# Kernel tuning notes

Measured on AMD Instinct MI355X. Metric: run time of the kernel, lower is better.

Reference implementation:

```python
import jax, jax.numpy as jnp
import numpy as np

B, T, D, H = 4, 2048, 1024, 16
HD = D // H  # head dim = 64


def setup_inputs() -> dict:
    key = jax.random.key(0)
    ks = jax.random.split(key, 6)
    s = 0.02
    return {
        "x": jax.random.normal(ks[0], (B, T, D), dtype=jnp.float32),
        "Wk": jax.random.normal(ks[1], (D, D), dtype=jnp.float32) * s,
        "Wq": jax.random.normal(ks[2], (D, D), dtype=jnp.float32) * s,
        "Wv": jax.random.normal(ks[3], (D, D), dtype=jnp.float32) * s,
        "Wp": jax.random.normal(ks[4], (D, D), dtype=jnp.float32) * s,
        "bp": jnp.zeros((D,), dtype=jnp.float32),
    }


def reference(x, Wk, Wq, Wv, Wp, bp):
    # nn.Linear applies x @ W.T; weights here are stored torch-style [out, in]
    Bq, Tq, _ = x.shape
    k = (x @ Wk.T).reshape(Bq, Tq, H, HD).transpose(0, 2, 1, 3)  # [B,H,T,hd]
    q = (x @ Wq.T).reshape(Bq, Tq, H, HD).transpose(0, 2, 1, 3)
    v = (x @ Wv.T).reshape(Bq, Tq, H, HD).transpose(0, 2, 1, 3)
    scale = HD ** -0.5
    attn = jnp.einsum('bhqd,bhkd->bhqk', q, k) * scale  # [B,H,T,T]
    causal = jnp.tril(jnp.ones((Tq, Tq), dtype=bool))
    attn = jnp.where(causal, attn, -jnp.inf)
    attn = jax.nn.softmax(attn, axis=-1)
    # dropout p=0.0 -> identity (eval semantics)
    out = jnp.einsum('bhqk,bhkd->bhqd', attn, v)  # [B,H,T,hd]
    out = out.transpose(0, 2, 1, 3).reshape(Bq, Tq, D)
    return out @ Wp.T + bp
```

## Files before the change

### kernel.cpp

```cpp
#include <hip/hip_runtime.h>
#include <hip/hip_bf16.h>
#include <stdint.h>


typedef __bf16 bf16x8 __attribute__((ext_vector_type(8)));
typedef float floatx4 __attribute__((ext_vector_type(4)));
typedef unsigned short ushort_t;
typedef unsigned short ushortx8 __attribute__((ext_vector_type(8)));
typedef unsigned short ushortx4 __attribute__((ext_vector_type(4)));

#define MFMA16(a, b, c) __builtin_amdgcn_mfma_f32_16x16x32_bf16((a), (b), (c), 0, 0, 0)

static __device__ __forceinline__ ushort_t f2bfu(float f) {
  union { float f; unsigned u; } v; v.f = f;
  unsigned r = v.u + 0x7FFFu + ((v.u >> 16) & 1u);
  return (ushort_t)(r >> 16);
}

static __device__ __forceinline__ void gl_lds16(const void* g, void* l) {
  __builtin_amdgcn_global_load_lds(
      (const __attribute__((address_space(1))) void*)g,
      (__attribute__((address_space(3))) void*)l, 16, 0, 0);
}

__global__ void cvt_kernel(const float* __restrict__ in, ushort_t* __restrict__ out, int n4) {
  int i = blockIdx.x * blockDim.x + threadIdx.x;
  if (i >= n4) return;
  const float4 f = reinterpret_cast<const float4*>(in)[i];
  ushortx4 o;
  o[0] = f2bfu(f.x); o[1] = f2bfu(f.y); o[2] = f2bfu(f.z); o[3] = f2bfu(f.w);
  reinterpret_cast<ushortx4*>(out)[i] = o;
}

__global__ __launch_bounds__(256) void gemm_qkv(
    const ushort_t* __restrict__ X,
    const ushort_t* __restrict__ Wq, const ushort_t* __restrict__ Wk,
    const ushort_t* __restrict__ Wv,
    ushort_t* __restrict__ qb, ushort_t* __restrict__ kb, ushort_t* __restrict__ vtb)
{
  const int z = blockIdx.z;
  const ushort_t* Bm = (z == 0) ? Wq : (z == 1) ? Wk : Wv;
  __shared__ ushort_t Al[128 * 64];
  __shared__ ushort_t Bl[128 * 64];
  const int tid = threadIdx.x;
  const int w = tid >> 6, lane = tid & 63, g = lane >> 4, c = lane & 15;
  const int wm = w >> 1, wn = w & 1;
  const int cswz = c & 7;
  const int m0 = blockIdx.x * 128, n0 = blockIdx.y * 128;

  floatx4 acc[4][4];
  const floatx4 zero4 = {0.f, 0.f, 0.f, 0.f};
#pragma unroll
  for (int i = 0; i < 4; ++i)
#pragma unroll
    for (int j = 0; j < 4; ++j) acc[i][j] = zero4;

  const int srow = tid >> 3;
  const int gsw  = ((tid & 7) ^ (srow & 7)) * 8;

  for (int k0 = 0; k0 < 1024; k0 += 64) {
#pragma unroll
    for (int p = 0; p < 4; ++p) {
      const int row = p * 32 + srow;
      gl_lds16(&X [(size_t)(m0 + row) * 1024 + k0 + gsw], &Al[p * 2048 + tid * 8]);
      gl_lds16(&Bm[(size_t)(n0 + row) * 1024 + k0 + gsw], &Bl[p * 2048 + tid * 8]);
    }
    __syncthreads();
#pragma unroll
    for (int kk = 0; kk < 2; ++kk) {
      bf16x8 af[4], bfr[4];
#pragma unroll
      for (int i = 0; i < 4; ++i) {
        const int sw = ((kk * 4 + g) ^ cswz) * 8;
        af[i]  = *reinterpret_cast<const bf16x8*>(&Al[(wm * 64 + i * 16 + c) * 64 + sw]);
        bfr[i] = *reinterpret_cast<const bf16x8*>(&Bl[(wn * 64 + i * 16 + c) * 64 + sw]);
      }
#pragma unroll
      for (int i = 0; i < 4; ++i)
#pragma unroll
        for (int j = 0; j < 4; ++j)
          acc[i][j] = MFMA16(af[i], bfr[j], acc[i][j]);
    }
    __syncthreads();
  }

#pragma unroll
  for (int i = 0; i < 4; ++i) {
#pragma unroll
    for (int j = 0; j < 4; ++j) {
      const int mbase = m0 + wm * 64 + i * 16 + g * 4;
      const int n = n0 + wn * 64 + j * 16 + c;
      const int h = n >> 6, d = n & 63;
      if (z == 2) {
        const int bb = mbase >> 11, t = mbase & 2047;
        ushortx4 pk;
#pragma unroll
        for (int r = 0; r < 4; ++r) pk[r] = f2bfu(acc[i][j][r]);
        *reinterpret_cast<ushortx4*>(&vtb[(size_t)((bb * 16 + h) * 64 + d) * 2048 + t]) = pk;
      } else {
        ushort_t* ob = (z == 0) ? qb : kb;
#pragma unroll
        for (int r = 0; r < 4; ++r) {
          const int m = mbase + r;
          const int bb = m >> 11, t = m & 2047;
          ob[(size_t)((bb * 16 + h) * 2048 + t) * 64 + d] = f2bfu(acc[i][j][r]);
        }
      }
    }
  }
}

__global__ __launch_bounds__(256) void attn_kernel(
    const ushort_t* __restrict__ qbuf, const ushort_t* __restrict__ kbuf,
    const ushort_t* __restrict__ vtbuf, ushort_t* __restrict__ obuf)
{
  const int j = blockIdx.x, h = blockIdx.y, b = blockIdx.z;
  const int tid = threadIdx.x, w = tid >> 6, lane = tid & 63, g = lane >> 4, c = lane & 15;
  const int cswz = c & 7;

  __shared__ ushort_t Kl[64 * 64];
  __shared__ ushort_t Vl[64 * 64];
  __shared__ ushort_t Pl[4][2][16 * 72];

  const size_t bh = (size_t)(b * 16 + h);
  const ushort_t* kb_bh = kbuf + bh * 2048 * 64;
  const ushort_t* vt_bh = vtbuf + bh * 64 * 2048;

  const int rb0 = j * 64 + w * 16;
  const int rb1 = (31 - j) * 64 + w * 16;

  bf16x8 aq0[2], aq1[2];
  {
    const ushort_t* qp0 = qbuf + (bh * 2048 + rb0 + c) * 64;
    aq0[0] = *reinterpret_cast<const bf16x8*>(qp0 + g * 8);
    aq0[1] = *reinterpret_cast<const bf16x8*>(qp0 + 32 + g * 8);
    const ushort_t* qp1 = qbuf + (bh * 2048 + rb1 + c) * 64;
    aq1[0] = *reinterpret_cast<const bf16x8*>(qp1 + g * 8);
    aq1[1] = *reinterpret_cast<const bf16x8*>(qp1 + 32 + g * 8);
  }

  floatx4 oacc0[4], oacc1[4];
  float lp0[4], lp1[4];
  const floatx4 zero4 = {0.f, 0.f, 0.f, 0.f};
#pragma unroll
  for (int td = 0; td < 4; ++td) { oacc0[td] = zero4; oacc1[td] = zero4; }
#pragma unroll
  for (int r = 0; r < 4; ++r) { lp0[r] = 0.f; lp1[r] = 0.f; }

  const int drow = tid >> 3;
  const int gsw  = ((tid & 7) ^ (drow & 7)) * 8;

  const int ktlast = 31 - j;
  for (int kt = 0; kt <= ktlast; ++kt) {
    const int key0 = kt * 64;
#pragma unroll
    for (int p = 0; p < 2; ++p) {
      const int r = p * 32 + drow;
      gl_lds16(&kb_bh[(size_t)(key0 + r) * 64 + gsw], &Kl[p * 2048 + tid * 8]);
      gl_lds16(&vt_bh[(size_t)r * 2048 + key0 + gsw], &Vl[p * 2048 + tid * 8]);
    }
    __syncthreads();

#pragma unroll
    for (int grp = 0; grp < 2; ++grp) {
      if (grp == 0 && kt > j) continue;
      const int rb = (grp == 0) ? rb0 : rb1;
      const int dg = (grp == 0) ? j : 31 - j;
      const bf16x8 a0 = (grp == 0) ? aq0[0] : aq1[0];
      const bf16x8 a1 = (grp == 0) ? aq0[1] : aq1[1];
      float pv[4][4];
#pragma unroll
      for (int t4 = 0; t4 < 4; ++t4) {
        const int krow = (t4 * 16 + c) * 64;
        const bf16x8 k0f = *reinterpret_cast<const bf16x8*>(&Kl[krow + ((g) ^ cswz) * 8]);
        const bf16x8 k1f = *reinterpret_cast<const bf16x8*>(&Kl[krow + ((4 + g) ^ cswz) * 8]);
        floatx4 sa = zero4;
        sa = MFMA16(a0, k0f, sa);
        sa = MFMA16(a1, k1f, sa);
        if (kt == dg) {
          const int key = key0 + t4 * 16 + c;
#pragma unroll
          for (int r = 0; r < 4; ++r) {
            const float e = __expf(sa[r] * 0.125f);
            pv[t4][r] = (key <= rb + g * 4 + r) ? e : 0.f;
          }
        } else {
#pragma unroll
          for (int r = 0; r < 4; ++r) pv[t4][r] = __expf(sa[r] * 0.125f);
        }
      }
#pragma unroll
      for (int r = 0; r < 4; ++r) {
        const float s = (pv[0][r] + pv[1][r]) + (pv[2][r] + pv[3][r]);
        if (grp == 0) lp0[r] += s; else lp1[r] += s;
      }

      ushort_t* pw = Pl[w][grp];
#pragma unroll
      for (int t4 = 0; t4 < 4; ++t4)
#pragma unroll
        for (int r = 0; r < 4; ++r)
          pw[(g * 4 + r) * 72 + t4 * 16 + c] = f2bfu(pv[t4][r]);
      const bf16x8 ap0 = *reinterpret_cast<const bf16x8*>(&pw[c * 72 + g * 8]);
      const bf16x8 ap1 = *reinterpret_cast<const bf16x8*>(&pw[c * 72 + 32 + g * 8]);
#pragma unroll
      for (int td = 0; td < 4; ++td) {
        const int vrow = (td * 16 + c) * 64;
        const bf16x8 bv0 = *reinterpret_cast<const bf16x8*>(&Vl[vrow + ((g) ^ cswz) * 8]);
        const bf16x8 bv1 = *reinterpret_cast<const bf16x8*>(&Vl[vrow + ((4 + g) ^ cswz) * 8]);
        if (grp == 0) {
          oacc0[td] = MFMA16(ap0, bv0, oacc0[td]);
          oacc0[td] = MFMA16(ap1, bv1, oacc0[td]);
        } else {
          oacc1[td] = MFMA16(ap0, bv0, oacc1[td]);
          oacc1[td] = MFMA16(ap1, bv1, oacc1[td]);
        }
      }
    }
    __syncthreads();
  }

#pragma unroll
  for (int grp = 0; grp < 2; ++grp) {
    const int rb = (grp == 0) ? rb0 : rb1;
#pragma unroll
    for (int r = 0; r < 4; ++r) {
      float ls = (grp == 0) ? lp0[r] : lp1[r];
#pragma unroll
      for (int o = 1; o < 16; o <<= 1) ls += __shfl_xor(ls, o, 64);
      const float inv = 1.f / ls;
      const int q = rb + g * 4 + r;
#pragma unroll
      for (int td = 0; td < 4; ++td) {
        const int d = td * 16 + c;
        const float ov = ((grp == 0) ? oacc0[td][r] : oacc1[td][r]) * inv;
        obuf[((size_t)(b * 2048 + q) * 16 + h) * 64 + d] = f2bfu(ov);
      }
    }
  }
}

__global__ __launch_bounds__(256) void gemm_proj(
    const ushort_t* __restrict__ A, const ushort_t* __restrict__ Wp,
    const float* __restrict__ bias, float* __restrict__ out)
{
  __shared__ ushort_t Al[128 * 64];
  __shared__ ushort_t Bl[128 * 64];
  const int tid = threadIdx.x;
  const int w = tid >> 6, lane = tid & 63, g = lane >> 4, c = lane & 15;
  const int wm = w >> 1, wn = w & 1;
  const int cswz = c & 7;
  const int m0 = blockIdx.x * 128, n0 = blockIdx.y * 128;

  floatx4 acc[4][4];
  const floatx4 zero4 = {0.f, 0.f, 0.f, 0.f};
#pragma unroll
  for (int i = 0; i < 4; ++i)
#pragma unroll
    for (int j = 0; j < 4; ++j) acc[i][j] = zero4;

  const int srow = tid >> 3;
  const int gsw  = ((tid & 7) ^ (srow & 7)) * 8;

  for (int k0 = 0; k0 < 1024; k0 += 64) {
#pragma unroll
    for (int p = 0; p < 4; ++p) {
      const int row = p * 32 + srow;
      gl_lds16(&A [(size_t)(m0 + row) * 1024 + k0 + gsw], &Al[p * 2048 + tid * 8]);
      gl_lds16(&Wp[(size_t)(n0 + row) * 1024 + k0 + gsw], &Bl[p * 2048 + tid * 8]);
    }
    __syncthreads();
#pragma unroll
    for (int kk = 0; kk < 2; ++kk) {
      bf16x8 af[4], bfr[4];
#pragma unroll
      for (int i = 0; i < 4; ++i) {
        const int sw = ((kk * 4 + g) ^ cswz) * 8;
        af[i]  = *reinterpret_cast<const bf16x8*>(&Al[(wm * 64 + i * 16 + c) * 64 + sw]);
        bfr[i] = *reinterpret_cast<const bf16x8*>(&Bl[(wn * 64 + i * 16 + c) * 64 + sw]);
      }
#pragma unroll
      for (int i = 0; i < 4; ++i)
#pragma unroll
        for (int j = 0; j < 4; ++j)
          acc[i][j] = MFMA16(af[i], bfr[j], acc[i][j]);
    }
    __syncthreads();
  }

#pragma unroll
  for (int i = 0; i < 4; ++i) {
#pragma unroll
    for (int j = 0; j < 4; ++j) {
      const int n = n0 + wn * 64 + j * 16 + c;
      const float bv = bias[n];
#pragma unroll
      for (int r = 0; r < 4; ++r) {
        const int m = m0 + wm * 64 + i * 16 + g * 4 + r;
        out[(size_t)m * 1024 + n] = acc[i][j][r] + bv;
      }
    }
  }
}

extern "C" void kernel_launch(void* const* d_in, const int* in_sizes, int n_in,
                              void* d_out, int out_size, void* d_ws, size_t ws_size,
                              hipStream_t stream) {
  const float* x  = (const float*)d_in[0];
  const float* Wk = (const float*)d_in[1];
  const float* Wq = (const float*)d_in[2];
  const float* Wv = (const float*)d_in[3];
  const float* Wp = (const float*)d_in[4];
  const float* bp = (const float*)d_in[5];
  float* out = (float*)d_out;

  char* ws = (char*)d_ws;
  const size_t SZ_X = (size_t)8192 * 1024 * 2;
  const size_t SZ_W = (size_t)1024 * 1024 * 2;
  ushort_t* xb    = (ushort_t*)ws;  ws += SZ_X;
  ushort_t* wkb   = (ushort_t*)ws;  ws += SZ_W;
  ushort_t* wqb   = (ushort_t*)ws;  ws += SZ_W;
  ushort_t* wvb   = (ushort_t*)ws;  ws += SZ_W;
  ushort_t* wpb   = (ushort_t*)ws;  ws += SZ_W;
  ushort_t* qbuf  = (ushort_t*)ws;  ws += SZ_X;
  ushort_t* kbuf  = (ushort_t*)ws;  ws += SZ_X;
  ushort_t* vtbuf = (ushort_t*)ws;  ws += SZ_X;
  ushort_t* obuf  = xb;

  cvt_kernel<<<8192, 256, 0, stream>>>(x,  xb,  8192 * 1024 / 4);
  cvt_kernel<<<1024, 256, 0, stream>>>(Wk, wkb, 1024 * 1024 / 4);
  cvt_kernel<<<1024, 256, 0, stream>>>(Wq, wqb, 1024 * 1024 / 4);
  cvt_kernel<<<1024, 256, 0, stream>>>(Wv, wvb, 1024 * 1024 / 4);
  cvt_kernel<<<1024, 256, 0, stream>>>(Wp, wpb, 1024 * 1024 / 4);

  gemm_qkv<<<dim3(64, 8, 3), 256, 0, stream>>>(xb, wqb, wkb, wvb, qbuf, kbuf, vtbuf);
  attn_kernel<<<dim3(16, 16, 4), 256, 0, stream>>>(qbuf, kbuf, vtbuf, obuf);
  gemm_proj<<<dim3(64, 8), 256, 0, stream>>>(obuf, wpb, bp, out);
}
```

Baseline: 280.6 us.

## Fuse conversions, widen attention key tiles, store Q transposed, truncate P

The five float-to-bf16 conversion launches become one kernel that writes into the contiguous workspace. The attention loop now stages 128-key K/V tiles per barrier instead of 64, which halves the number of synchronizations, and it shares a single P scratch buffer per wave. Q is written transposed by the QKV GEMM with vectorized stores and gathered element-wise in attention. P is converted to bf16 by truncation rather than rounding, which slightly reduces accuracy, and the larger tiles use more LDS.

```diff
diff --git a/kernel.cpp b/kernel.cpp
--- a/kernel.cpp
+++ b/kernel.cpp
@@ -16,6 +16,10 @@
   unsigned r = v.u + 0x7FFFu + ((v.u >> 16) & 1u);
   return (ushort_t)(r >> 16);
 }
+static __device__ __forceinline__ ushort_t f2bfu_trunc(float f) {
+  union { float f; unsigned u; } v; v.f = f;
+  return (ushort_t)(v.u >> 16);
+}
 
 static __device__ __forceinline__ void gl_lds16(const void* g, void* l) {
   __builtin_amdgcn_global_load_lds(
@@ -23,20 +27,29 @@
       (__attribute__((address_space(3))) void*)l, 16, 0, 0);
 }
 
-__global__ void cvt_kernel(const float* __restrict__ in, ushort_t* __restrict__ out, int n4) {
-  int i = blockIdx.x * blockDim.x + threadIdx.x;
-  if (i >= n4) return;
-  const float4 f = reinterpret_cast<const float4*>(in)[i];
+__global__ void cvt_all(const float* __restrict__ x,  const float* __restrict__ wk,
+                        const float* __restrict__ wq, const float* __restrict__ wv,
+                        const float* __restrict__ wp, ushortx4* __restrict__ dst) {
+  const int i = blockIdx.x * blockDim.x + threadIdx.x;
+  const float4* src; int off;
+  if (i < 2097152) { src = (const float4*)x; off = i; }
+  else {
+    const int r = i - 2097152;
+    const int sel = r >> 18;
+    off = r & 262143;
+    src = (const float4*)(sel == 0 ? wk : sel == 1 ? wq : sel == 2 ? wv : wp);
+  }
+  const float4 f = src[off];
   ushortx4 o;
   o[0] = f2bfu(f.x); o[1] = f2bfu(f.y); o[2] = f2bfu(f.z); o[3] = f2bfu(f.w);
-  reinterpret_cast<ushortx4*>(out)[i] = o;
+  dst[i] = o;
 }
 
 __global__ __launch_bounds__(256) void gemm_qkv(
     const ushort_t* __restrict__ X,
     const ushort_t* __restrict__ Wq, const ushort_t* __restrict__ Wk,
     const ushort_t* __restrict__ Wv,
-    ushort_t* __restrict__ qb, ushort_t* __restrict__ kb, ushort_t* __restrict__ vtb)
+    ushort_t* __restrict__ qtb, ushort_t* __restrict__ kb, ushort_t* __restrict__ vtb)
 {
   const int z = blockIdx.z;
   const ushort_t* Bm = (z == 0) ? Wq : (z == 1) ? Wk : Wv;
@@ -91,19 +104,19 @@
       const int mbase = m0 + wm * 64 + i * 16 + g * 4;
       const int n = n0 + wn * 64 + j * 16 + c;
       const int h = n >> 6, d = n & 63;
-      if (z == 2) {
+      if (z != 1) {
+        ushort_t* ob = (z == 0) ? qtb : vtb;
         const int bb = mbase >> 11, t = mbase & 2047;
         ushortx4 pk;
 #pragma unroll
         for (int r = 0; r < 4; ++r) pk[r] = f2bfu(acc[i][j][r]);
-        *reinterpret_cast<ushortx4*>(&vtb[(size_t)((bb * 16 + h) * 64 + d) * 2048 + t]) = pk;
+        *reinterpret_cast<ushortx4*>(&ob[(size_t)((bb * 16 + h) * 64 + d) * 2048 + t]) = pk;
       } else {
-        ushort_t* ob = (z == 0) ? qb : kb;
 #pragma unroll
         for (int r = 0; r < 4; ++r) {
           const int m = mbase + r;
           const int bb = m >> 11, t = m & 2047;
-          ob[(size_t)((bb * 16 + h) * 2048 + t) * 64 + d] = f2bfu(acc[i][j][r]);
+          kb[(size_t)((bb * 16 + h) * 2048 + t) * 64 + d] = f2bfu(acc[i][j][r]);
         }
       }
     }
@@ -111,32 +124,36 @@
 }
 
 __global__ __launch_bounds__(256) void attn_kernel(
-    const ushort_t* __restrict__ qbuf, const ushort_t* __restrict__ kbuf,
+    const ushort_t* __restrict__ qtbuf, const ushort_t* __restrict__ kbuf,
     const ushort_t* __restrict__ vtbuf, ushort_t* __restrict__ obuf)
 {
   const int j = blockIdx.x, h = blockIdx.y, b = blockIdx.z;
   const int tid = threadIdx.x, w = tid >> 6, lane = tid & 63, g = lane >> 4, c = lane & 15;
-  const int cswz = c & 7;
-
-  __shared__ ushort_t Kl[64 * 64];
-  __shared__ ushort_t Vl[64 * 64];
-  __shared__ ushort_t Pl[4][2][16 * 72];
+
+  __shared__ ushort_t Kl[128 * 64];
+  __shared__ ushort_t Vl[64 * 128];
+  __shared__ ushort_t Pl[4][16 * 72];
 
   const size_t bh = (size_t)(b * 16 + h);
   const ushort_t* kb_bh = kbuf + bh * 2048 * 64;
   const ushort_t* vt_bh = vtbuf + bh * 64 * 2048;
+  const ushort_t* qt_bh = qtbuf + bh * 64 * 2048;
 
   const int rb0 = j * 64 + w * 16;
   const int rb1 = (31 - j) * 64 + w * 16;
 
   bf16x8 aq0[2], aq1[2];
   {
-    const ushort_t* qp0 = qbuf + (bh * 2048 + rb0 + c) * 64;
-    aq0[0] = *reinterpret_cast<const bf16x8*>(qp0 + g * 8);
-    aq0[1] = *reinterpret_cast<const bf16x8*>(qp0 + 32 + g * 8);
-    const ushort_t* qp1 = qbuf + (bh * 2048 + rb1 + c) * 64;
-    aq1[0] = *reinterpret_cast<const bf16x8*>(qp1 + g * 8);
-    aq1[1] = *reinterpret_cast<const bf16x8*>(qp1 + 32 + g * 8);
+    union { ushortx8 u; bf16x8 v; } t00, t01, t10, t11;
+#pragma unroll
+    for (int jj = 0; jj < 8; ++jj) {
+      const int d0 = g * 8 + jj, d1 = 32 + g * 8 + jj;
+      t00.u[jj] = qt_bh[(size_t)d0 * 2048 + rb0 + c];
+      t01.u[jj] = qt_bh[(size_t)d1 * 2048 + rb0 + c];
+      t10.u[jj] = qt_bh[(size_t)d0 * 2048 + rb1 + c];
+      t11.u[jj] = qt_bh[(size_t)d1 * 2048 + rb1 + c];
+    }
+    aq0[0] = t00.v; aq0[1] = t01.v; aq1[0] = t10.v; aq1[1] = t11.v;
   }
 
   floatx4 oacc0[4], oacc1[4];
@@ -147,73 +164,82 @@
 #pragma unroll
   for (int r = 0; r < 4; ++r) { lp0[r] = 0.f; lp1[r] = 0.f; }
 
-  const int drow = tid >> 3;
-  const int gsw  = ((tid & 7) ^ (drow & 7)) * 8;
-
-  const int ktlast = 31 - j;
-  for (int kt = 0; kt <= ktlast; ++kt) {
-    const int key0 = kt * 64;
-#pragma unroll
-    for (int p = 0; p < 2; ++p) {
-      const int r = p * 32 + drow;
-      gl_lds16(&kb_bh[(size_t)(key0 + r) * 64 + gsw], &Kl[p * 2048 + tid * 8]);
-      gl_lds16(&vt_bh[(size_t)r * 2048 + key0 + gsw], &Vl[p * 2048 + tid * 8]);
-    }
-    __syncthreads();
-
-#pragma unroll
-    for (int grp = 0; grp < 2; ++grp) {
-      if (grp == 0 && kt > j) continue;
-      const int rb = (grp == 0) ? rb0 : rb1;
-      const int dg = (grp == 0) ? j : 31 - j;
-      const bf16x8 a0 = (grp == 0) ? aq0[0] : aq1[0];
-      const bf16x8 a1 = (grp == 0) ? aq0[1] : aq1[1];
-      float pv[4][4];
-#pragma unroll
-      for (int t4 = 0; t4 < 4; ++t4) {
-        const int krow = (t4 * 16 + c) * 64;
-        const bf16x8 k0f = *reinterpret_cast<const bf16x8*>(&Kl[krow + ((g) ^ cswz) * 8]);
-        const bf16x8 k1f = *reinterpret_cast<const bf16x8*>(&Kl[krow + ((4 + g) ^ cswz) * 8]);
-        floatx4 sa = zero4;
-        sa = MFMA16(a0, k0f, sa);
-        sa = MFMA16(a1, k1f, sa);
-        if (kt == dg) {
-          const int key = key0 + t4 * 16 + c;
-#pragma unroll
-          for (int r = 0; r < 4; ++r) {
-            const float e = __expf(sa[r] * 0.125f);
-            pv[t4][r] = (key <= rb + g * 4 + r) ? e : 0.f;
+  const int krow_s = tid >> 3;
+  const int kgsw   = ((tid & 7) ^ (krow_s & 7)) * 8;
+  const int vrow_s = tid >> 4;
+  const int vgsw   = ((tid & 15) ^ (vrow_s & 15)) * 8;
+
+  const int n128 = (33 - j) >> 1;
+  for (int kt = 0; kt < n128; ++kt) {
+    const int key0 = kt * 128;
+#pragma unroll
+    for (int p = 0; p < 4; ++p) {
+      const int kr = p * 32 + krow_s;
+      gl_lds16(&kb_bh[(size_t)(key0 + kr) * 64 + kgsw], &Kl[p * 2048 + tid * 8]);
+      const int vr = p * 16 + vrow_s;
+      gl_lds16(&vt_bh[(size_t)vr * 2048 + key0 + vgsw], &Vl[p * 2048 + tid * 8]);
+    }
+    __syncthreads();
+
+#pragma unroll
+    for (int s = 0; s < 2; ++s) {
+      const int ti = 2 * kt + s;
+      const int key0s = ti * 64;
+#pragma unroll
+      for (int grp = 0; grp < 2; ++grp) {
+        const int lim = (grp == 0) ? j : 31 - j;
+        if (ti > lim) continue;
+        const int rb = (grp == 0) ? rb0 : rb1;
+        const bf16x8 a0 = (grp == 0) ? aq0[0] : aq1[0];
+        const bf16x8 a1 = (grp == 0) ? aq0[1] : aq1[1];
+
+        float pv[4][4];
+#pragma unroll
+        for (int t4 = 0; t4 < 4; ++t4) {
+          const int krow = s * 64 + t4 * 16 + c;
+          const bf16x8 k0f = *reinterpret_cast<const bf16x8*>(&Kl[krow * 64 + ((g) ^ (c & 7)) * 8]);
+          const bf16x8 k1f = *reinterpret_cast<const bf16x8*>(&Kl[krow * 64 + ((4 + g) ^ (c & 7)) * 8]);
+          floatx4 sa = zero4;
+          sa = MFMA16(a0, k0f, sa);
+          sa = MFMA16(a1, k1f, sa);
+          if (ti == lim) {
+            const int key = key0s + t4 * 16 + c;
+#pragma unroll
+            for (int r = 0; r < 4; ++r) {
+              const float e = __expf(sa[r] * 0.125f);
+              pv[t4][r] = (key <= rb + g * 4 + r) ? e : 0.f;
+            }
+          } else {
+#pragma unroll
+            for (int r = 0; r < 4; ++r) pv[t4][r] = __expf(sa[r] * 0.125f);
           }
-        } else {
-#pragma unroll
-          for (int r = 0; r < 4; ++r) pv[t4][r] = __expf(sa[r] * 0.125f);
         }
-      }
-#pragma unroll
-      for (int r = 0; r < 4; ++r) {
-        const float s = (pv[0][r] + pv[1][r]) + (pv[2][r] + pv[3][r]);
-        if (grp == 0) lp0[r] += s; else lp1[r] += s;
-      }
-
-      ushort_t* pw = Pl[w][grp];
-#pragma unroll
-      for (int t4 = 0; t4 < 4; ++t4)
-#pragma unroll
-        for (int r = 0; r < 4; ++r)
-          pw[(g * 4 + r) * 72 + t4 * 16 + c] = f2bfu(pv[t4][r]);
-      const bf16x8 ap0 = *reinterpret_cast<const bf16x8*>(&pw[c * 72 + g * 8]);
-      const bf16x8 ap1 = *reinterpret_cast<const bf16x8*>(&pw[c * 72 + 32 + g * 8]);
-#pragma unroll
-      for (int td = 0; td < 4; ++td) {
-        const int vrow = (td * 16 + c) * 64;
-        const bf16x8 bv0 = *reinterpret_cast<const bf16x8*>(&Vl[vrow + ((g) ^ cswz) * 8]);
-        const bf16x8 bv1 = *reinterpret_cast<const bf16x8*>(&Vl[vrow + ((4 + g) ^ cswz) * 8]);
-        if (grp == 0) {
-          oacc0[td] = MFMA16(ap0, bv0, oacc0[td]);
-          oacc0[td] = MFMA16(ap1, bv1, oacc0[td]);
-        } else {
-          oacc1[td] = MFMA16(ap0, bv0, oacc1[td]);
-          oacc1[td] = MFMA16(ap1, bv1, oacc1[td]);
+#pragma unroll
+        for (int r = 0; r < 4; ++r) {
+          const float sm = (pv[0][r] + pv[1][r]) + (pv[2][r] + pv[3][r]);
+          if (grp == 0) lp0[r] += sm; else lp1[r] += sm;
+        }
+
+        ushort_t* pw = Pl[w];
+#pragma unroll
+        for (int t4 = 0; t4 < 4; ++t4)
+#pragma unroll
+          for (int r = 0; r < 4; ++r)
+            pw[(g * 4 + r) * 72 + t4 * 16 + c] = f2bfu_trunc(pv[t4][r]);
+        const bf16x8 ap0 = *reinterpret_cast<const bf16x8*>(&pw[c * 72 + g * 8]);
+        const bf16x8 ap1 = *reinterpret_cast<const bf16x8*>(&pw[c * 72 + 32 + g * 8]);
+#pragma unroll
+        for (int td = 0; td < 4; ++td) {
+          const int vrow = td * 16 + c;
+          const bf16x8 bv0 = *reinterpret_cast<const bf16x8*>(&Vl[vrow * 128 + ((s * 8 + g) ^ c) * 8]);
+          const bf16x8 bv1 = *reinterpret_cast<const bf16x8*>(&Vl[vrow * 128 + ((s * 8 + 4 + g) ^ c) * 8]);
+          if (grp == 0) {
+            oacc0[td] = MFMA16(ap0, bv0, oacc0[td]);
+            oacc0[td] = MFMA16(ap1, bv1, oacc0[td]);
+          } else {
+            oacc1[td] = MFMA16(ap0, bv0, oacc1[td]);
+            oacc1[td] = MFMA16(ap1, bv1, oacc1[td]);
+          }
         }
       }
     }
@@ -322,18 +348,14 @@
   ushort_t* wqb   = (ushort_t*)ws;  ws += SZ_W;
   ushort_t* wvb   = (ushort_t*)ws;  ws += SZ_W;
   ushort_t* wpb   = (ushort_t*)ws;  ws += SZ_W;
-  ushort_t* qbuf  = (ushort_t*)ws;  ws += SZ_X;
+  ushort_t* qtbuf = (ushort_t*)ws;  ws += SZ_X;
   ushort_t* kbuf  = (ushort_t*)ws;  ws += SZ_X;
   ushort_t* vtbuf = (ushort_t*)ws;  ws += SZ_X;
   ushort_t* obuf  = xb;
 
-  cvt_kernel<<<8192, 256, 0, stream>>>(x,  xb,  8192 * 1024 / 4);
-  cvt_kernel<<<1024, 256, 0, stream>>>(Wk, wkb, 1024 * 1024 / 4);
-  cvt_kernel<<<1024, 256, 0, stream>>>(Wq, wqb, 1024 * 1024 / 4);
-  cvt_kernel<<<1024, 256, 0, stream>>>(Wv, wvb, 1024 * 1024 / 4);
-  cvt_kernel<<<1024, 256, 0, stream>>>(Wp, wpb, 1024 * 1024 / 4);
-
-  gemm_qkv<<<dim3(64, 8, 3), 256, 0, stream>>>(xb, wqb, wkb, wvb, qbuf, kbuf, vtbuf);
-  attn_kernel<<<dim3(16, 16, 4), 256, 0, stream>>>(qbuf, kbuf, vtbuf, obuf);
+  cvt_all<<<12288, 256, 0, stream>>>(x, Wk, Wq, Wv, Wp, (ushortx4*)xb);
+
+  gemm_qkv<<<dim3(64, 8, 3), 256, 0, stream>>>(xb, wqb, wkb, wvb, qtbuf, kbuf, vtbuf);
+  attn_kernel<<<dim3(16, 16, 4), 256, 0, stream>>>(qtbuf, kbuf, vtbuf, obuf);
   gemm_proj<<<dim3(64, 8), 256, 0, stream>>>(obuf, wpb, bp, out);
 }
```

Result: faster. 266.9 us (-4.9%).
